# Kernel optimization log

Measured on AMD Instinct MI355X. Metric: run time of the kernel, lower is better.

The kernel has to match this reference:

```python
import jax, jax.numpy as jnp
import numpy as np

SEG = 8  # conv1d groups


def _grouped_mix(y, W2, b2, seg):
    # y: [b, C_in, L]; W2: [C_out, C_in//seg]; grouped 1x1 conv1d
    b_, cin, L = y.shape
    cout = W2.shape[0]
    yg = y.reshape(b_, seg, cin // seg, L)
    Wg = W2.reshape(seg, cout // seg, cin // seg)
    z = jnp.einsum('bgcl,goc->bgol', yg, Wg).reshape(b_, cout, L)
    return z + b2[None, :, None]


def _mix_h(x, W1, b1, W2, b2):
    # x: [b,h,w,d]
    b_, H, Wd, D = x.shape
    y = jnp.einsum('bhwd,ed->bhwe', x, W1) + b1            # 1x1 conv2d -> [b,h,w,e]
    y = jnp.transpose(y, (0, 3, 1, 2)).reshape(b_, -1, Wd)  # 'b d h w -> b (d h) w'
    z = _grouped_mix(y, W2, b2, SEG)                        # [b, h*h, w]
    attn = jax.nn.softmax(
        z.reshape(b_, H, H, Wd).transpose(0, 3, 1, 2), axis=-1)  # [b,w,h1,h2]
    xr = jnp.transpose(x, (0, 2, 1, 3))                     # [b,w,h,d]
    out = jnp.einsum('bwij,bwjd->bwid', attn, xr)
    return jnp.transpose(out, (0, 2, 1, 3))                 # [b,h,w,d]


def _mix_w(x, W1, b1, W2, b2):
    # x: [b,h,w,d]
    b_, H, Wd, D = x.shape
    y = jnp.einsum('bhwd,ed->bhwe', x, W1) + b1             # [b,h,w,e]
    y = jnp.transpose(y, (0, 3, 2, 1)).reshape(b_, -1, H)   # 'b d w h -> b (d w) h'
    z = _grouped_mix(y, W2, b2, SEG)                        # [b, w*w, h]
    attn = jax.nn.softmax(
        z.reshape(b_, Wd, Wd, H).transpose(0, 3, 1, 2), axis=-1)  # [b,h,w1,w2]
    return jnp.einsum('bhij,bhjd->bhid', attn, x)           # [b,h,w,d]


def setup_inputs() -> dict:
    key = jax.random.key(0)
    ks = jax.random.split(key, 16)
    B, H, W, D, E = 64, 32, 32, 384, 2
    s = 0.05
    return {
        'x':   jax.random.normal(ks[0], (B, H, W, D), jnp.float32),
        'Wc':  jax.random.normal(ks[1], (D, D), jnp.float32) * s,
        'bc':  jnp.zeros((D,), jnp.float32),
        'Wo':  jax.random.normal(ks[2], (D, D), jnp.float32) * s,
        'bo':  jnp.zeros((D,), jnp.float32),
        'W1h': jax.random.normal(ks[3], (E, D), jnp.float32) * s,
        'b1h': jnp.zeros((E,), jnp.float32),
        'W2h': jax.random.normal(ks[4], (H * H, E * H // SEG), jnp.float32) * s,
        'b2h': jnp.zeros((H * H,), jnp.float32),
        'W1w': jax.random.normal(ks[5], (E, D), jnp.float32) * s,
        'b1w': jnp.zeros((E,), jnp.float32),
        'W2w': jax.random.normal(ks[6], (W * W, E * W // SEG), jnp.float32) * s,
        'b2w': jnp.zeros((W * W,), jnp.float32),
    }


def reference(x, Wc, bc, Wo, bo, W1h, b1h, W2h, b2h, W1w, b1w, W2w, b2w):
    Y_c = jnp.einsum('bhwd,od->bhwo', x, Wc) + bc
    Y_h = _mix_h(x, W1h, b1h, W2h, b2h)
    Y_w = _mix_w(x, W1w, b1w, W2w, b2w)
    Y = Y_h + Y_w + Y_c
    return jnp.einsum('bhwd,od->bhwo', Y, Wo) + bo
```

## Files before the change

### kernel.cpp

```cpp
#include <hip/hip_runtime.h>
#include <hip/hip_bf16.h>
#include <cstdint>
#include <cstddef>

typedef __bf16 bf16;
typedef __attribute__((ext_vector_type(8))) __bf16 bf16x8;
typedef __attribute__((ext_vector_type(4))) float floatx4;

#define NPIX 65536

__global__ void k_prep_w(const float* __restrict__ Wc, const float* __restrict__ bc,
                         const float* __restrict__ Wo, const float* __restrict__ bo,
                         bf16* __restrict__ Wfull, float* __restrict__ bco) {
    int blk = blockIdx.x;
    int t = threadIdx.x;
    if (blk < 384) {
        int o = blk;
        float acc = 0.f;
        for (int d = 0; d < 384; ++d)
            acc += Wo[o * 384 + d] * Wc[d * 384 + t];
        Wfull[(size_t)o * 768 + t]       = (bf16)Wo[o * 384 + t];
        Wfull[(size_t)o * 768 + 384 + t] = (bf16)acc;
    } else {
        int o = t;
        float acc = bo[o];
        for (int d = 0; d < 384; ++d)
            acc += Wo[o * 384 + d] * bc[d];
        bco[o] = acc;
    }
}

__global__ void k_proj(const float* __restrict__ xf, bf16* __restrict__ xb,
                       const float* __restrict__ W1h, const float* __restrict__ b1h,
                       const float* __restrict__ W1w, const float* __restrict__ b1w,
                       float* __restrict__ yh, float* __restrict__ yw) {
    int t  = threadIdx.x;
    int lg = t & 7;
    int pg = t >> 3;
    int p  = blockIdx.x * 32 + pg;
    int b = p >> 10, h = (p >> 5) & 31, w = p & 31;
    const float4* xp4 = (const float4*)(xf + (size_t)p * 384);
    float a0 = 0.f, a1 = 0.f, a2 = 0.f, a3 = 0.f;
#pragma unroll
    for (int j = 0; j < 6; ++j) {
        int c = j * 8 + lg;
        float4 xa = xp4[c * 2], xcv = xp4[c * 2 + 1];
        bf16x8 v;
        v[0] = (bf16)xa.x; v[1] = (bf16)xa.y; v[2] = (bf16)xa.z; v[3] = (bf16)xa.w;
        v[4] = (bf16)xcv.x; v[5] = (bf16)xcv.y; v[6] = (bf16)xcv.z; v[7] = (bf16)xcv.w;
        *(bf16x8*)(xb + (size_t)p * 384 + c * 8) = v;
        const float4* h0 = (const float4*)(W1h + c * 8);
        const float4* h1 = (const float4*)(W1h + 384 + c * 8);
        const float4* w0 = (const float4*)(W1w + c * 8);
        const float4* w1 = (const float4*)(W1w + 384 + c * 8);
        float4 h0a = h0[0], h0b = h0[1], h1a = h1[0], h1b = h1[1];
        float4 w0a = w0[0], w0b = w0[1], w1a = w1[0], w1b = w1[1];
        a0 += xa.x*h0a.x + xa.y*h0a.y + xa.z*h0a.z + xa.w*h0a.w
            + xcv.x*h0b.x + xcv.y*h0b.y + xcv.z*h0b.z + xcv.w*h0b.w;
        a1 += xa.x*h1a.x + xa.y*h1a.y + xa.z*h1a.z + xa.w*h1a.w
            + xcv.x*h1b.x + xcv.y*h1b.y + xcv.z*h1b.z + xcv.w*h1b.w;
        a2 += xa.x*w0a.x + xa.y*w0a.y + xa.z*w0a.z + xa.w*w0a.w
            + xcv.x*w0b.x + xcv.y*w0b.y + xcv.z*w0b.z + xcv.w*w0b.w;
        a3 += xa.x*w1a.x + xa.y*w1a.y + xa.z*w1a.z + xa.w*w1a.w
            + xcv.x*w1b.x + xcv.y*w1b.y + xcv.z*w1b.z + xcv.w*w1b.w;
    }
#pragma unroll
    for (int m = 1; m < 8; m <<= 1) {
        a0 += __shfl_xor(a0, m, 64);
        a1 += __shfl_xor(a1, m, 64);
        a2 += __shfl_xor(a2, m, 64);
        a3 += __shfl_xor(a3, m, 64);
    }
    if (lg == 0) {
        yh[((b * 2 + 0) * 32 + h) * 32 + w] = a0 + b1h[0];
        yh[((b * 2 + 1) * 32 + h) * 32 + w] = a1 + b1h[1];
        yw[((b * 2 + 0) * 32 + w) * 32 + h] = a2 + b1w[0];
        yw[((b * 2 + 1) * 32 + w) * 32 + h] = a3 + b1w[1];
    }
}

__global__ void k_attn(const float* __restrict__ yproj,
                       const float* __restrict__ W2, const float* __restrict__ b2,
                       bf16* __restrict__ attn) {
    int blk = blockIdx.x;
    int bi = blk >> 5, r1 = blk & 31;
    int g = r1 >> 2;
    int cb = g * 8;
    int e = cb >> 5, rb = cb & 31;
    int lane = threadIdx.x;
    int l = lane & 31, half = lane >> 5;
    float yv[8];
    const float* ybase = yproj + (((bi * 2 + e) * 32 + rb) * 32 + l);
#pragma unroll
    for (int c = 0; c < 8; ++c) yv[c] = ybase[c * 32];
    float z[16];
#pragma unroll
    for (int jj = 0; jj < 16; ++jj) {
        int r2 = half * 16 + jj;
        int row = r1 * 32 + r2;
        const float4* wp = (const float4*)(W2 + (size_t)row * 8);
        float4 wa = wp[0], wb = wp[1];
        z[jj] = b2[row]
              + yv[0]*wa.x + yv[1]*wa.y + yv[2]*wa.z + yv[3]*wa.w
              + yv[4]*wb.x + yv[5]*wb.y + yv[6]*wb.z + yv[7]*wb.w;
    }
    float m = -1e30f;
#pragma unroll
    for (int jj = 0; jj < 16; ++jj) m = fmaxf(m, z[jj]);
    m = fmaxf(m, __shfl_xor(m, 32, 64));
    float s = 0.f;
#pragma unroll
    for (int jj = 0; jj < 16; ++jj) { z[jj] = __expf(z[jj] - m); s += z[jj]; }
    s += __shfl_xor(s, 32, 64);
    float inv = 1.f / s;
    bf16x8 o0, o1;
#pragma unroll
    for (int jj = 0; jj < 8; ++jj) o0[jj] = (bf16)(z[jj] * inv);
#pragma unroll
    for (int jj = 0; jj < 8; ++jj) o1[jj] = (bf16)(z[8 + jj] * inv);
    bf16x8* dst = (bf16x8*)(attn + ((((size_t)bi * 32 + l) * 32 + r1) * 32 + half * 16));
    dst[0] = o0;
    dst[1] = o1;
}

__global__ __launch_bounds__(256) void k_mix(const bf16* __restrict__ x,
                                             const bf16* __restrict__ attn_h,
                                             const bf16* __restrict__ attn_w,
                                             bf16* __restrict__ T) {
    __shared__ float Ts[1024 * 16];
    int c  = blockIdx.x;
    int bi = blockIdx.y;
    int dbase = c * 16;
    int tid = threadIdx.x;
    int wv = tid >> 6, lane = tid & 63;
    int n16 = lane & 15, quad = lane >> 4;
    int dcol = dbase + n16;

    for (int wl = 0; wl < 8; ++wl) {
        int w = wv * 8 + wl;
        const bf16* abase = attn_h + ((size_t)(bi * 32 + w) * 32) * 32;
        bf16x8 af0 = *(const bf16x8*)(abase + (n16) * 32 + quad * 8);
        bf16x8 af1 = *(const bf16x8*)(abase + (16 + n16) * 32 + quad * 8);
        bf16x8 bfrag;
#pragma unroll
        for (int i = 0; i < 8; ++i) {
            int j = quad * 8 + i;
            bfrag[i] = x[((size_t)(bi * 32 + j) * 32 + w) * 384 + dcol];
        }
        floatx4 c0 = {0.f, 0.f, 0.f, 0.f}, c1 = {0.f, 0.f, 0.f, 0.f};
        c0 = __builtin_amdgcn_mfma_f32_16x16x32_bf16(af0, bfrag, c0, 0, 0, 0);
        c1 = __builtin_amdgcn_mfma_f32_16x16x32_bf16(af1, bfrag, c1, 0, 0, 0);
#pragma unroll
        for (int r = 0; r < 4; ++r) {
            int h0 = quad * 4 + r;
            Ts[(h0 * 32 + w) * 16 + n16]        = c0[r];
            Ts[((16 + h0) * 32 + w) * 16 + n16] = c1[r];
        }
    }
    __syncthreads();
    for (int hl = 0; hl < 8; ++hl) {
        int h = wv * 8 + hl;
        const bf16* abase = attn_w + ((size_t)(bi * 32 + h) * 32) * 32;
        const bf16* xr = x + ((size_t)(bi * 32 + h) * 32) * 384;
        bf16* Tr = T + ((size_t)(bi * 32 + h) * 32) * 384;
        bf16x8 af0 = *(const bf16x8*)(abase + (n16) * 32 + quad * 8);
        bf16x8 af1 = *(const bf16x8*)(abase + (16 + n16) * 32 + quad * 8);
        bf16x8 bfrag;
#pragma unroll
        for (int i = 0; i < 8; ++i) {
            int j = quad * 8 + i;
            bfrag[i] = xr[(size_t)j * 384 + dcol];
        }
        floatx4 c0 = {0.f, 0.f, 0.f, 0.f}, c1 = {0.f, 0.f, 0.f, 0.f};
        c0 = __builtin_amdgcn_mfma_f32_16x16x32_bf16(af0, bfrag, c0, 0, 0, 0);
        c1 = __builtin_amdgcn_mfma_f32_16x16x32_bf16(af1, bfrag, c1, 0, 0, 0);
#pragma unroll
        for (int r = 0; r < 4; ++r) {
            int w0 = quad * 4 + r;
            Tr[(size_t)w0 * 384 + dcol]        = (bf16)(c0[r] + Ts[(h * 32 + w0) * 16 + n16]);
            Tr[(size_t)(16 + w0) * 384 + dcol] = (bf16)(c1[r] + Ts[(h * 32 + (16 + w0)) * 16 + n16]);
        }
    }
}

#define LDP 72
__global__ __launch_bounds__(256) void k_gemm(const bf16* __restrict__ T, const bf16* __restrict__ x,
                                              const bf16* __restrict__ Wfull, const float* __restrict__ bco,
                                              float* __restrict__ out) {
    __shared__ bf16 As[128 * LDP];
    __shared__ bf16 Bs[128 * LDP];
    int bx = blockIdx.x;
    int gid = (bx & 7) * 192 + (bx >> 3);
    int nt = gid % 3, pt = gid / 3;
    int obase = nt * 128;
    int pbase = pt * 128;
    int tid = threadIdx.x;
    int wv = tid >> 6, lane = tid & 63;
    int wm = wv & 1, wn = wv >> 1;
    int n16 = lane & 15, quad = lane >> 4;
    int lrow = tid >> 3;
    int lchunk = tid & 7;
    floatx4 zero = {0.f, 0.f, 0.f, 0.f};
    floatx4 acc[4][4];
#pragma unroll
    for (int i = 0; i < 4; ++i)
#pragma unroll
        for (int j = 0; j < 4; ++j) acc[i][j] = zero;

    for (int kt = 0; kt < 12; ++kt) {
        const bf16* Asrc = (kt < 6) ? (T + (size_t)pbase * 384 + kt * 64)
                                    : (x + (size_t)pbase * 384 + (kt - 6) * 64);
        const bf16* Bsrc = Wfull + (size_t)obase * 768 + kt * 64;
        bf16x8 av[4], bv[4];
#pragma unroll
        for (int s = 0; s < 4; ++s)
            av[s] = *(const bf16x8*)(Asrc + (size_t)(s * 32 + lrow) * 384 + lchunk * 8);
#pragma unroll
        for (int s = 0; s < 4; ++s)
            bv[s] = *(const bf16x8*)(Bsrc + (size_t)(s * 32 + lrow) * 768 + lchunk * 8);
        __syncthreads();
#pragma unroll
        for (int s = 0; s < 4; ++s)
            *(bf16x8*)(As + (s * 32 + lrow) * LDP + lchunk * 8) = av[s];
#pragma unroll
        for (int s = 0; s < 4; ++s)
            *(bf16x8*)(Bs + (s * 32 + lrow) * LDP + lchunk * 8) = bv[s];
        __syncthreads();
#pragma unroll
        for (int ks = 0; ks < 2; ++ks) {
            bf16x8 a[4], b[4];
#pragma unroll
            for (int i = 0; i < 4; ++i)
                a[i] = *(const bf16x8*)(As + (wm * 64 + i * 16 + n16) * LDP + ks * 32 + quad * 8);
#pragma unroll
            for (int i = 0; i < 4; ++i)
                b[i] = *(const bf16x8*)(Bs + (wn * 64 + i * 16 + n16) * LDP + ks * 32 + quad * 8);
#pragma unroll
            for (int i = 0; i < 4; ++i)
#pragma unroll
                for (int j = 0; j < 4; ++j)
                    acc[i][j] = __builtin_amdgcn_mfma_f32_16x16x32_bf16(a[i], b[j], acc[i][j], 0, 0, 0);
        }
    }
#pragma unroll
    for (int j = 0; j < 4; ++j) {
        int o = obase + wn * 64 + j * 16 + n16;
        float bcv = bco[o];
#pragma unroll
        for (int i = 0; i < 4; ++i) {
            int prow = pbase + wm * 64 + i * 16 + quad * 4;
#pragma unroll
            for (int r = 0; r < 4; ++r)
                out[(size_t)(prow + r) * 384 + o] = acc[i][j][r] + bcv;
        }
    }
}

extern "C" void kernel_launch(void* const* d_in, const int* in_sizes, int n_in,
                              void* d_out, int out_size, void* d_ws, size_t ws_size,
                              hipStream_t stream) {
    const float* x   = (const float*)d_in[0];
    const float* Wc  = (const float*)d_in[1];
    const float* bc  = (const float*)d_in[2];
    const float* Wo  = (const float*)d_in[3];
    const float* bo  = (const float*)d_in[4];
    const float* W1h = (const float*)d_in[5];
    const float* b1h = (const float*)d_in[6];
    const float* W2h = (const float*)d_in[7];
    const float* b2h = (const float*)d_in[8];
    const float* W1w = (const float*)d_in[9];
    const float* b1w = (const float*)d_in[10];
    const float* W2w = (const float*)d_in[11];
    const float* b2w = (const float*)d_in[12];
    float* out = (float*)d_out;

    char* ws = (char*)d_ws;
    size_t off = 0;
    auto alloc = [&](size_t bytes) {
        void* p = ws + off;
        off = (off + bytes + 255) & ~(size_t)255;
        return p;
    };
    bf16*  xb     = (bf16*)alloc((size_t)NPIX * 384 * 2);
    float* yh     = (float*)alloc((size_t)131072 * 4);
    float* yw     = (float*)alloc((size_t)131072 * 4);
    bf16*  attn_h = (bf16*)alloc((size_t)2097152 * 2);
    bf16*  attn_w = (bf16*)alloc((size_t)2097152 * 2);
    bf16*  T      = (bf16*)alloc((size_t)NPIX * 384 * 2);
    bf16*  Wfull  = (bf16*)alloc((size_t)384 * 768 * 2);
    float* bco    = (float*)alloc((size_t)384 * 4);

    hipLaunchKernelGGL(k_prep_w, dim3(385), dim3(384), 0, stream, Wc, bc, Wo, bo, Wfull, bco);
    hipLaunchKernelGGL(k_proj, dim3(2048), dim3(256), 0, stream, x, xb, W1h, b1h, W1w, b1w, yh, yw);
    hipLaunchKernelGGL(k_attn, dim3(2048), dim3(64), 0, stream, yh, W2h, b2h, attn_h);
    hipLaunchKernelGGL(k_attn, dim3(2048), dim3(64), 0, stream, yw, W2w, b2w, attn_w);
    hipLaunchKernelGGL(k_mix, dim3(24, 64), dim3(256), 0, stream, xb, attn_h, attn_w, T);
    hipLaunchKernelGGL(k_gemm, dim3(1536), dim3(256), 0, stream, T, xb, Wfull, bco, out);
}
```

Baseline: 372.6 us.

## Stage x tile in LDS via async global_load_lds and remap k_mix blocks

k_mix now first copies its 1024x16 bf16 slice of x into shared memory with async global-to-LDS 16-byte copies, then reads both the h-mix and w-mix B fragments from LDS instead of issuing scattered 2-byte global loads. The intermediate Ts buffer shrinks from float to bf16, which halves its LDS footprint and may allow more blocks per CU. The grid becomes 1D with a swizzled block-to-(batch, channel-chunk) mapping, apparently to improve cache locality. Storing the intermediate in bf16 adds a second rounding step and slightly reduces accuracy.

```diff
diff --git a/kernel.cpp b/kernel.cpp
--- a/kernel.cpp
+++ b/kernel.cpp
@@ -8,6 +8,12 @@
 typedef __attribute__((ext_vector_type(4))) float floatx4;
 
 #define NPIX 65536
+
+__device__ inline void async_copy16(void* lds, const void* g) {
+    __builtin_amdgcn_global_load_lds(
+        (const __attribute__((address_space(1))) void*)g,
+        (__attribute__((address_space(3))) void*)lds, 16, 0, 0);
+}
 
 __global__ void k_prep_w(const float* __restrict__ Wc, const float* __restrict__ bc,
                          const float* __restrict__ Wo, const float* __restrict__ bo,
@@ -127,58 +133,75 @@
                                              const bf16* __restrict__ attn_h,
                                              const bf16* __restrict__ attn_w,
                                              bf16* __restrict__ T) {
-    __shared__ float Ts[1024 * 16];
-    int c  = blockIdx.x;
-    int bi = blockIdx.y;
+    __shared__ bf16 Xs[1024 * 16];
+    __shared__ bf16 Ts[1024 * 16];
+    int n = blockIdx.x;
+    int a = n >> 5, r = n & 31;
+    int q = a * 8 + (r & 7);
+    int bi = q / 6, cq = q % 6;
+    int c = cq * 4 + (r >> 3);
     int dbase = c * 16;
     int tid = threadIdx.x;
     int wv = tid >> 6, lane = tid & 63;
     int n16 = lane & 15, quad = lane >> 4;
-    int dcol = dbase + n16;
-
+
+    const char* gbase = (const char*)(x + (size_t)bi * 1024 * 384 + dbase);
+#pragma unroll
+    for (int it = 0; it < 8; ++it) {
+        int p0 = wv * 256 + it * 32;
+        const char* g = gbase + (size_t)(p0 + (lane >> 1)) * 768 + (lane & 1) * 16;
+        char* l = (char*)Xs + p0 * 32 + lane * 16;
+        async_copy16(l, g);
+    }
+    __syncthreads();
+
+#pragma unroll
     for (int wl = 0; wl < 8; ++wl) {
         int w = wv * 8 + wl;
-        const bf16* abase = attn_h + ((size_t)(bi * 32 + w) * 32) * 32;
-        bf16x8 af0 = *(const bf16x8*)(abase + (n16) * 32 + quad * 8);
-        bf16x8 af1 = *(const bf16x8*)(abase + (16 + n16) * 32 + quad * 8);
+        const bf16* ab = attn_h + ((size_t)(bi * 32 + w) * 32) * 32;
+        bf16x8 af0 = *(const bf16x8*)(ab + n16 * 32 + quad * 8);
+        bf16x8 af1 = *(const bf16x8*)(ab + (16 + n16) * 32 + quad * 8);
         bf16x8 bfrag;
 #pragma unroll
         for (int i = 0; i < 8; ++i) {
             int j = quad * 8 + i;
-            bfrag[i] = x[((size_t)(bi * 32 + j) * 32 + w) * 384 + dcol];
+            bfrag[i] = Xs[(j * 32 + w) * 16 + n16];
         }
         floatx4 c0 = {0.f, 0.f, 0.f, 0.f}, c1 = {0.f, 0.f, 0.f, 0.f};
         c0 = __builtin_amdgcn_mfma_f32_16x16x32_bf16(af0, bfrag, c0, 0, 0, 0);
         c1 = __builtin_amdgcn_mfma_f32_16x16x32_bf16(af1, bfrag, c1, 0, 0, 0);
 #pragma unroll
-        for (int r = 0; r < 4; ++r) {
-            int h0 = quad * 4 + r;
-            Ts[(h0 * 32 + w) * 16 + n16]        = c0[r];
-            Ts[((16 + h0) * 32 + w) * 16 + n16] = c1[r];
+        for (int rr = 0; rr < 4; ++rr) {
+            int h0 = quad * 4 + rr;
+            Ts[(h0 * 32 + w) * 16 + n16]        = (bf16)c0[rr];
+            Ts[((16 + h0) * 32 + w) * 16 + n16] = (bf16)c1[rr];
         }
     }
     __syncthreads();
+
+#pragma unroll
     for (int hl = 0; hl < 8; ++hl) {
         int h = wv * 8 + hl;
-        const bf16* abase = attn_w + ((size_t)(bi * 32 + h) * 32) * 32;
-        const bf16* xr = x + ((size_t)(bi * 32 + h) * 32) * 384;
-        bf16* Tr = T + ((size_t)(bi * 32 + h) * 32) * 384;
-        bf16x8 af0 = *(const bf16x8*)(abase + (n16) * 32 + quad * 8);
-        bf16x8 af1 = *(const bf16x8*)(abase + (16 + n16) * 32 + quad * 8);
+        const bf16* ab = attn_w + ((size_t)(bi * 32 + h) * 32) * 32;
+        bf16x8 af0 = *(const bf16x8*)(ab + n16 * 32 + quad * 8);
+        bf16x8 af1 = *(const bf16x8*)(ab + (16 + n16) * 32 + quad * 8);
         bf16x8 bfrag;
 #pragma unroll
         for (int i = 0; i < 8; ++i) {
             int j = quad * 8 + i;
-            bfrag[i] = xr[(size_t)j * 384 + dcol];
+            bfrag[i] = Xs[(h * 32 + j) * 16 + n16];
         }
         floatx4 c0 = {0.f, 0.f, 0.f, 0.f}, c1 = {0.f, 0.f, 0.f, 0.f};
         c0 = __builtin_amdgcn_mfma_f32_16x16x32_bf16(af0, bfrag, c0, 0, 0, 0);
         c1 = __builtin_amdgcn_mfma_f32_16x16x32_bf16(af1, bfrag, c1, 0, 0, 0);
-#pragma unroll
-        for (int r = 0; r < 4; ++r) {
-            int w0 = quad * 4 + r;
-            Tr[(size_t)w0 * 384 + dcol]        = (bf16)(c0[r] + Ts[(h * 32 + w0) * 16 + n16]);
-            Tr[(size_t)(16 + w0) * 384 + dcol] = (bf16)(c1[r] + Ts[(h * 32 + (16 + w0)) * 16 + n16]);
+        bf16* Tr = T + ((size_t)(bi * 32 + h) * 32) * 384 + dbase;
+#pragma unroll
+        for (int rr = 0; rr < 4; ++rr) {
+            int w0 = quad * 4 + rr;
+            Tr[(size_t)w0 * 384 + n16] =
+                (bf16)(c0[rr] + (float)Ts[(h * 32 + w0) * 16 + n16]);
+            Tr[(size_t)(16 + w0) * 384 + n16] =
+                (bf16)(c1[rr] + (float)Ts[(h * 32 + 16 + w0) * 16 + n16]);
         }
     }
 }
@@ -294,6 +317,6 @@
     hipLaunchKernelGGL(k_proj, dim3(2048), dim3(256), 0, stream, x, xb, W1h, b1h, W1w, b1w, yh, yw);
     hipLaunchKernelGGL(k_attn, dim3(2048), dim3(64), 0, stream, yh, W2h, b2h, attn_h);
     hipLaunchKernelGGL(k_attn, dim3(2048), dim3(64), 0, stream, yw, W2w, b2w, attn_w);
-    hipLaunchKernelGGL(k_mix, dim3(24, 64), dim3(256), 0, stream, xb, attn_h, attn_w, T);
+    hipLaunchKernelGGL(k_mix, dim3(1536), dim3(256), 0, stream, xb, attn_h, attn_w, T);
     hipLaunchKernelGGL(k_gemm, dim3(1536), dim3(256), 0, stream, T, xb, Wfull, bco, out);
 }
```

Result: faster. 324.9 us (-12.8%).
